# Kernel optimization log

Hardware: AMD Instinct MI355X
Metric: run time of the kernel (lower is better)

Reference implementation:

```python
import jax, jax.numpy as jnp
import numpy as np

EPS = 1e-12  # guard sqrt at zero distance


def setup_inputs() -> dict:
    key = jax.random.key(0)
    k1, k2 = jax.random.split(key)
    B, C, N = 4, 3, 8192
    predict_pc = jax.random.normal(k1, (B, C, N), dtype=jnp.float32)
    gt_pc = jax.random.normal(k2, (B, C, N), dtype=jnp.float32)
    return {"predict_pc": predict_pc, "gt_pc": gt_pc}


def reference(predict_pc, gt_pc):
    # predict_pc: [B, 3, Np], gt_pc: [B, 3, Ng]
    B = gt_pc.shape[0]
    Np = predict_pc.shape[2]
    Ng = gt_pc.shape[2]
    denom = B * (Ng + Np)

    # Pairwise Euclidean distances d[b, n, m] = ||predict[b,:,n] - gt[b,:,m]||
    # via the |p|^2 + |g|^2 - 2 p.g expansion (avoids [B,3,Np,Ng] intermediate).
    p2 = jnp.sum(predict_pc * predict_pc, axis=1)            # [B, Np]
    g2 = jnp.sum(gt_pc * gt_pc, axis=1)                      # [B, Ng]
    dot = jnp.einsum('bcn,bcm->bnm', predict_pc, gt_pc)      # [B, Np, Ng]
    d2 = p2[:, :, None] + g2[:, None, :] - 2.0 * dot         # [B, Np, Ng]
    d = jnp.sqrt(jnp.maximum(d2, EPS))

    # z: for each gt point, distance to nearest predicted point -> min over Np
    z = jnp.min(d, axis=1)   # [B, Ng]
    # z_2: for each predicted point, distance to nearest gt point -> min over Ng
    z2 = jnp.min(d, axis=2)  # [B, Np]

    loss = z.sum() / denom + z2.sum() / denom
    return loss
```

## Files before the change

kernel.cpp:

```cpp
#include <hip/hip_runtime.h>
#include <math.h>


#define B_       4
#define N_       8192
#define THREADS  256
#define RX       8
#define XB       (THREADS * RX)
#define XBLKS    (N_ / XB)
#define YSPLITS  32
#define YCHUNK   (N_ / YSPLITS)
#define NGROUPS  (2 * B_ * XBLKS)
#define POISON   0xAAAAAAAAu

typedef float v2f __attribute__((ext_vector_type(2)));

__device__ __forceinline__ v2f pk_fma(v2f a, v2f b, v2f c) {
    v2f d;
    asm("v_pk_fma_f32 %0, %1, %2, %3" : "=v"(d) : "v"(a), "v"(b), "v"(c));
    return d;
}


__global__ __launch_bounds__(THREADS)
void chamfer_fused_kernel(const float* __restrict__ P, const float* __restrict__ G,
                          unsigned* __restrict__ mins, unsigned* __restrict__ gcnt,
                          unsigned* __restrict__ fcnt, float* __restrict__ gsum,
                          float* __restrict__ out)
{
    __shared__ float4 ytile[2 * (YCHUNK / 2)];
    __shared__ float red[THREADS];
    __shared__ unsigned s_ticket;

    const int t      = threadIdx.x;
    const int xblk   = blockIdx.x;
    const int ysplit = blockIdx.y;
    const int bz     = blockIdx.z;
    const int pass   = bz >> 2;
    const int b      = bz & 3;
    const int gid    = bz * XBLKS + xblk;

    const float* Xb = (pass ? G : P) + (size_t)b * 3 * N_;
    const float* Yb = (pass ? P : G) + (size_t)b * 3 * N_;

    const int ybase = ysplit * YCHUNK;
    if (t < YCHUNK / 2) {
        const int n0 = ybase + 2 * t;
        float2 x01 = *(const float2*)&Yb[n0];
        float2 y01 = *(const float2*)&Yb[N_ + n0];
        float2 z01 = *(const float2*)&Yb[2 * N_ + n0];
        float w0 = fmaf(x01.x, x01.x, fmaf(y01.x, y01.x, z01.x * z01.x));
        float w1 = fmaf(x01.y, x01.y, fmaf(y01.y, y01.y, z01.y * z01.y));
        ytile[2 * t]     = make_float4(x01.x, x01.y, y01.x, y01.y);
        ytile[2 * t + 1] = make_float4(z01.x, z01.y, w0, w1);
    }

    const int xbase = xblk * XB;
    v2f m2x2[RX], m2y2[RX], m2z2[RX];
    float p2[RX], mn[RX];
#pragma unroll
    for (int r = 0; r < RX; ++r) {
        const int n = xbase + r * THREADS + t;
        float px = Xb[n];
        float py = Xb[N_ + n];
        float pz = Xb[2 * N_ + n];
        p2[r]   = fmaf(px, px, fmaf(py, py, pz * pz));
        float ax = -2.0f * px, ay = -2.0f * py, az = -2.0f * pz;
        m2x2[r] = (v2f){ax, ax};
        m2y2[r] = (v2f){ay, ay};
        m2z2[r] = (v2f){az, az};
        mn[r]   = 3.4e38f;
    }
    __syncthreads();

#pragma unroll 2
    for (int jj = 0; jj < YCHUNK / 2; ++jj) {
        float4 a4 = ytile[2 * jj];
        float4 b4 = ytile[2 * jj + 1];
        v2f gx2 = (v2f){a4.x, a4.y};
        v2f gy2 = (v2f){a4.z, a4.w};
        v2f gz2 = (v2f){b4.x, b4.y};
        v2f gw2 = (v2f){b4.z, b4.w};
#pragma unroll
        for (int r = 0; r < RX; ++r) {
            v2f s = pk_fma(m2z2[r], gz2, gw2);
            s = pk_fma(m2y2[r], gy2, s);
            s = pk_fma(m2x2[r], gx2, s);
            mn[r] = fminf(fminf(mn[r], s.x), s.y);
        }
    }

    unsigned* mybase = mins + (size_t)(pass * B_ + b) * N_ + xbase;
#pragma unroll
    for (int r = 0; r < RX; ++r) {
        float v = fmaxf(mn[r] + p2[r], 1e-12f);
        atomicMin(&mybase[r * THREADS + t], __float_as_uint(v));
    }

    __syncthreads();
    if (t == 0) {
        __threadfence();
        s_ticket = atomicAdd(&gcnt[gid], 1u);
    }
    __syncthreads();
    if (s_ticket != POISON + (unsigned)(YSPLITS - 1)) return;

    __threadfence();
    const uint4* vmin = (const uint4*)(mins + (size_t)(pass * B_ + b) * N_ + xbase);
    uint4 q0 = vmin[t];
    uint4 q1 = vmin[THREADS + t];
    float a = sqrtf(__uint_as_float(q0.x)) + sqrtf(__uint_as_float(q0.y))
            + sqrtf(__uint_as_float(q0.z)) + sqrtf(__uint_as_float(q0.w))
            + sqrtf(__uint_as_float(q1.x)) + sqrtf(__uint_as_float(q1.y))
            + sqrtf(__uint_as_float(q1.z)) + sqrtf(__uint_as_float(q1.w));
    red[t] = a;
    __syncthreads();
    for (int off = 128; off > 0; off >>= 1) {
        if (t < off) red[t] += red[t + off];
        __syncthreads();
    }
    if (t == 0) {
        gsum[gid] = red[0];
        __threadfence();
        s_ticket = atomicAdd(fcnt, 1u);
    }
    __syncthreads();
    if (s_ticket != POISON + (unsigned)(NGROUPS - 1)) return;

    __threadfence();
    red[t] = (t < NGROUPS) ? gsum[t] : 0.0f;
    __syncthreads();
    for (int off = 128; off > 0; off >>= 1) {
        if (t < off) red[t] += red[t + off];
        __syncthreads();
    }
    if (t == 0) out[0] = red[0] * (1.0f / 65536.0f);
}

extern "C" void kernel_launch(void* const* d_in, const int* in_sizes, int n_in,
                              void* d_out, int out_size, void* d_ws, size_t ws_size,
                              hipStream_t stream)
{
    const float* P = (const float*)d_in[0];
    const float* G = (const float*)d_in[1];
    float* out = (float*)d_out;

    unsigned* w    = (unsigned*)d_ws;
    unsigned* mins = w;
    unsigned* gcnt = w + 65536;
    unsigned* fcnt = w + 65600;
    float*    gsum = (float*)(w + 65664);

    dim3 grid(XBLKS, YSPLITS, 2 * B_);
    chamfer_fused_kernel<<<grid, THREADS, 0, stream>>>(P, G, mins, gcnt, fcnt, gsum, out);
}
```

Baseline: 97.96 us.

## Split chamfer into pack, sweep, and reduce kernels with global-memory Y streaming

Adds a multi-kernel path: a pack kernel precomputes interleaved Y records with squared norms, a sweep kernel streams those records from global memory with register prefetch and fewer X points per thread, and writes per-split partial minima. Two reduction kernels then take minima, apply sqrt, and sum, replacing atomics and ticket counters. The fused atomic kernel remains as a fallback when the workspace is too small. This trades per-block LDS staging and atomics for more launches, a large partial buffer, and lower per-thread reuse.

```diff
diff --git a/kernel.cpp b/kernel.cpp
--- a/kernel.cpp
+++ b/kernel.cpp
@@ -5,13 +5,6 @@
 #define B_       4
 #define N_       8192
 #define THREADS  256
-#define RX       8
-#define XB       (THREADS * RX)
-#define XBLKS    (N_ / XB)
-#define YSPLITS  32
-#define YCHUNK   (N_ / YSPLITS)
-#define NGROUPS  (2 * B_ * XBLKS)
-#define POISON   0xAAAAAAAAu
 
 typedef float v2f __attribute__((ext_vector_type(2)));
 
@@ -21,45 +14,57 @@
     return d;
 }
 
-
-__global__ __launch_bounds__(THREADS)
-void chamfer_fused_kernel(const float* __restrict__ P, const float* __restrict__ G,
-                          unsigned* __restrict__ mins, unsigned* __restrict__ gcnt,
-                          unsigned* __restrict__ fcnt, float* __restrict__ gsum,
-                          float* __restrict__ out)
-{
-    __shared__ float4 ytile[2 * (YCHUNK / 2)];
-    __shared__ float red[THREADS];
-    __shared__ unsigned s_ticket;
-
+#define RX1      2
+#define XB1      (THREADS * RX1)
+#define XBLKS1   (N_ / XB1)
+#define YSPL1    16
+#define YREC     (N_ / 2 / YSPL1)
+#define NPB      (2 * B_)
+#define NREC_PB  (N_ / 2)
+
+#define OFF_PACKED   0
+#define OFF_PARTIAL  262144
+#define OFF_GSUM2    1310720
+#define WORDS_NEED   1310976
+
+__global__ __launch_bounds__(THREADS)
+void chamfer_pack_kernel(const float* __restrict__ P, const float* __restrict__ G,
+                         float4* __restrict__ packed)
+{
+    const int g  = blockIdx.x * THREADS + threadIdx.x;
+    const int pb = g >> 12;
+    const int j  = g & 4095;
+    const int pass = pb >> 2, b = pb & 3;
+    const float* Yb = (pass ? P : G) + (size_t)b * 3 * N_;
+    const int n0 = 2 * j;
+    float2 x01 = *(const float2*)&Yb[n0];
+    float2 y01 = *(const float2*)&Yb[N_ + n0];
+    float2 z01 = *(const float2*)&Yb[2 * N_ + n0];
+    float w0 = fmaf(x01.x, x01.x, fmaf(y01.x, y01.x, z01.x * z01.x));
+    float w1 = fmaf(x01.y, x01.y, fmaf(y01.y, y01.y, z01.y * z01.y));
+    packed[2 * (size_t)g]     = make_float4(x01.x, x01.y, y01.x, y01.y);
+    packed[2 * (size_t)g + 1] = make_float4(z01.x, z01.y, w0, w1);
+}
+
+__global__ __launch_bounds__(THREADS)
+void chamfer_sweep_kernel(const float* __restrict__ P, const float* __restrict__ G,
+                          const float4* __restrict__ packed,
+                          float* __restrict__ partial)
+{
     const int t      = threadIdx.x;
     const int xblk   = blockIdx.x;
     const int ysplit = blockIdx.y;
     const int bz     = blockIdx.z;
     const int pass   = bz >> 2;
     const int b      = bz & 3;
-    const int gid    = bz * XBLKS + xblk;
 
     const float* Xb = (pass ? G : P) + (size_t)b * 3 * N_;
-    const float* Yb = (pass ? P : G) + (size_t)b * 3 * N_;
-
-    const int ybase = ysplit * YCHUNK;
-    if (t < YCHUNK / 2) {
-        const int n0 = ybase + 2 * t;
-        float2 x01 = *(const float2*)&Yb[n0];
-        float2 y01 = *(const float2*)&Yb[N_ + n0];
-        float2 z01 = *(const float2*)&Yb[2 * N_ + n0];
-        float w0 = fmaf(x01.x, x01.x, fmaf(y01.x, y01.x, z01.x * z01.x));
-        float w1 = fmaf(x01.y, x01.y, fmaf(y01.y, y01.y, z01.y * z01.y));
-        ytile[2 * t]     = make_float4(x01.x, x01.y, y01.x, y01.y);
-        ytile[2 * t + 1] = make_float4(z01.x, z01.y, w0, w1);
-    }
-
-    const int xbase = xblk * XB;
-    v2f m2x2[RX], m2y2[RX], m2z2[RX];
-    float p2[RX], mn[RX];
-#pragma unroll
-    for (int r = 0; r < RX; ++r) {
+    const int xbase = xblk * XB1;
+
+    v2f m2x2[RX1], m2y2[RX1], m2z2[RX1];
+    float p2[RX1], mn[RX1];
+#pragma unroll
+    for (int r = 0; r < RX1; ++r) {
         const int n = xbase + r * THREADS + t;
         float px = Xb[n];
         float py = Xb[N_ + n];
@@ -71,10 +76,130 @@
         m2z2[r] = (v2f){az, az};
         mn[r]   = 3.4e38f;
     }
-    __syncthreads();
-
+
+    const float4* rec = packed + 2 * ((size_t)bz * NREC_PB + ysplit * YREC);
+    float4 a0 = rec[0], b0 = rec[1];
+    float4 a1 = rec[2], b1 = rec[3];
 #pragma unroll 2
-    for (int jj = 0; jj < YCHUNK / 2; ++jj) {
+    for (int jj = 0; jj < YREC; ++jj) {
+        float4 an = rec[2 * jj + 4];
+        float4 bn = rec[2 * jj + 5];
+        v2f gx2 = (v2f){a0.x, a0.y};
+        v2f gy2 = (v2f){a0.z, a0.w};
+        v2f gz2 = (v2f){b0.x, b0.y};
+        v2f gw2 = (v2f){b0.z, b0.w};
+#pragma unroll
+        for (int r = 0; r < RX1; ++r) {
+            v2f s = pk_fma(m2z2[r], gz2, gw2);
+            s = pk_fma(m2y2[r], gy2, s);
+            s = pk_fma(m2x2[r], gx2, s);
+            mn[r] = fminf(fminf(mn[r], s.x), s.y);
+        }
+        a0 = a1; b0 = b1; a1 = an; b1 = bn;
+    }
+
+    float* pout = partial + ((size_t)bz * YSPL1 + ysplit) * N_ + xbase;
+#pragma unroll
+    for (int r = 0; r < RX1; ++r)
+        pout[r * THREADS + t] = fmaxf(mn[r] + p2[r], 1e-12f);
+}
+
+__global__ __launch_bounds__(THREADS)
+void chamfer_reduce1_kernel(const float* __restrict__ partial,
+                            float* __restrict__ gsum2)
+{
+    __shared__ float red[THREADS];
+    const int g  = blockIdx.x * THREADS + threadIdx.x;
+    const int pb = g >> 13;
+    const int x  = g & 8191;
+    const float* p = partial + (size_t)pb * YSPL1 * N_ + x;
+    float m = p[0];
+#pragma unroll
+    for (int ys = 1; ys < YSPL1; ++ys)
+        m = fminf(m, p[(size_t)ys * N_]);
+    red[threadIdx.x] = sqrtf(m);
+    __syncthreads();
+    for (int off = 128; off > 0; off >>= 1) {
+        if (threadIdx.x < off) red[threadIdx.x] += red[threadIdx.x + off];
+        __syncthreads();
+    }
+    if (threadIdx.x == 0) gsum2[blockIdx.x] = red[0];
+}
+
+__global__ __launch_bounds__(THREADS)
+void chamfer_final_kernel(const float* __restrict__ gsum2, float* __restrict__ out)
+{
+    __shared__ float red[THREADS];
+    red[threadIdx.x] = gsum2[threadIdx.x];
+    __syncthreads();
+    for (int off = 128; off > 0; off >>= 1) {
+        if (threadIdx.x < off) red[threadIdx.x] += red[threadIdx.x + off];
+        __syncthreads();
+    }
+    if (threadIdx.x == 0) out[0] = red[0] * (1.0f / 65536.0f);
+}
+
+#define LRX      8
+#define LXB      (THREADS * LRX)
+#define LXBLKS   (N_ / LXB)
+#define LYSPL    32
+#define LYCHUNK  (N_ / LYSPL)
+#define LNGROUPS (2 * B_ * LXBLKS)
+#define POISON   0xAAAAAAAAu
+
+__global__ __launch_bounds__(THREADS)
+void chamfer_fused_kernel(const float* __restrict__ P, const float* __restrict__ G,
+                          unsigned* __restrict__ mins, unsigned* __restrict__ gcnt,
+                          unsigned* __restrict__ fcnt, float* __restrict__ gsum,
+                          float* __restrict__ out)
+{
+    __shared__ float4 ytile[2 * (LYCHUNK / 2)];
+    __shared__ float red[THREADS];
+    __shared__ unsigned s_ticket;
+
+    const int t      = threadIdx.x;
+    const int xblk   = blockIdx.x;
+    const int ysplit = blockIdx.y;
+    const int bz     = blockIdx.z;
+    const int pass   = bz >> 2;
+    const int b      = bz & 3;
+    const int gid    = bz * LXBLKS + xblk;
+
+    const float* Xb = (pass ? G : P) + (size_t)b * 3 * N_;
+    const float* Yb = (pass ? P : G) + (size_t)b * 3 * N_;
+
+    const int ybase = ysplit * LYCHUNK;
+    if (t < LYCHUNK / 2) {
+        const int n0 = ybase + 2 * t;
+        float2 x01 = *(const float2*)&Yb[n0];
+        float2 y01 = *(const float2*)&Yb[N_ + n0];
+        float2 z01 = *(const float2*)&Yb[2 * N_ + n0];
+        float w0 = fmaf(x01.x, x01.x, fmaf(y01.x, y01.x, z01.x * z01.x));
+        float w1 = fmaf(x01.y, x01.y, fmaf(y01.y, y01.y, z01.y * z01.y));
+        ytile[2 * t]     = make_float4(x01.x, x01.y, y01.x, y01.y);
+        ytile[2 * t + 1] = make_float4(z01.x, z01.y, w0, w1);
+    }
+
+    const int xbase = xblk * LXB;
+    v2f m2x2[LRX], m2y2[LRX], m2z2[LRX];
+    float p2[LRX], mn[LRX];
+#pragma unroll
+    for (int r = 0; r < LRX; ++r) {
+        const int n = xbase + r * THREADS + t;
+        float px = Xb[n];
+        float py = Xb[N_ + n];
+        float pz = Xb[2 * N_ + n];
+        p2[r]   = fmaf(px, px, fmaf(py, py, pz * pz));
+        float ax = -2.0f * px, ay = -2.0f * py, az = -2.0f * pz;
+        m2x2[r] = (v2f){ax, ax};
+        m2y2[r] = (v2f){ay, ay};
+        m2z2[r] = (v2f){az, az};
+        mn[r]   = 3.4e38f;
+    }
+    __syncthreads();
+
+#pragma unroll 2
+    for (int jj = 0; jj < LYCHUNK / 2; ++jj) {
         float4 a4 = ytile[2 * jj];
         float4 b4 = ytile[2 * jj + 1];
         v2f gx2 = (v2f){a4.x, a4.y};
@@ -82,7 +207,7 @@
         v2f gz2 = (v2f){b4.x, b4.y};
         v2f gw2 = (v2f){b4.z, b4.w};
 #pragma unroll
-        for (int r = 0; r < RX; ++r) {
+        for (int r = 0; r < LRX; ++r) {
             v2f s = pk_fma(m2z2[r], gz2, gw2);
             s = pk_fma(m2y2[r], gy2, s);
             s = pk_fma(m2x2[r], gx2, s);
@@ -92,7 +217,7 @@
 
     unsigned* mybase = mins + (size_t)(pass * B_ + b) * N_ + xbase;
 #pragma unroll
-    for (int r = 0; r < RX; ++r) {
+    for (int r = 0; r < LRX; ++r) {
         float v = fmaxf(mn[r] + p2[r], 1e-12f);
         atomicMin(&mybase[r * THREADS + t], __float_as_uint(v));
     }
@@ -103,7 +228,7 @@
         s_ticket = atomicAdd(&gcnt[gid], 1u);
     }
     __syncthreads();
-    if (s_ticket != POISON + (unsigned)(YSPLITS - 1)) return;
+    if (s_ticket != POISON + (unsigned)(LYSPL - 1)) return;
 
     __threadfence();
     const uint4* vmin = (const uint4*)(mins + (size_t)(pass * B_ + b) * N_ + xbase);
@@ -125,10 +250,10 @@
         s_ticket = atomicAdd(fcnt, 1u);
     }
     __syncthreads();
-    if (s_ticket != POISON + (unsigned)(NGROUPS - 1)) return;
+    if (s_ticket != POISON + (unsigned)(LNGROUPS - 1)) return;
 
     __threadfence();
-    red[t] = (t < NGROUPS) ? gsum[t] : 0.0f;
+    red[t] = (t < LNGROUPS) ? gsum[t] : 0.0f;
     __syncthreads();
     for (int off = 128; off > 0; off >>= 1) {
         if (t < off) red[t] += red[t + off];
@@ -145,12 +270,22 @@
     const float* G = (const float*)d_in[1];
     float* out = (float*)d_out;
 
-    unsigned* w    = (unsigned*)d_ws;
-    unsigned* mins = w;
-    unsigned* gcnt = w + 65536;
-    unsigned* fcnt = w + 65600;
-    float*    gsum = (float*)(w + 65664);
-
-    dim3 grid(XBLKS, YSPLITS, 2 * B_);
-    chamfer_fused_kernel<<<grid, THREADS, 0, stream>>>(P, G, mins, gcnt, fcnt, gsum, out);
-}
+    if (ws_size >= (size_t)WORDS_NEED * 4) {
+        float*  wsf     = (float*)d_ws;
+        float4* packed  = (float4*)(wsf + OFF_PACKED);
+        float*  partial = wsf + OFF_PARTIAL;
+        float*  gsum2   = wsf + OFF_GSUM2;
+        chamfer_pack_kernel<<<dim3(128), THREADS, 0, stream>>>(P, G, packed);
+        chamfer_sweep_kernel<<<dim3(XBLKS1, YSPL1, 2 * B_), THREADS, 0, stream>>>(P, G, packed, partial);
+        chamfer_reduce1_kernel<<<dim3(256), THREADS, 0, stream>>>(partial, gsum2);
+        chamfer_final_kernel<<<dim3(1), THREADS, 0, stream>>>(gsum2, out);
+    } else {
+        unsigned* w    = (unsigned*)d_ws;
+        unsigned* mins = w;
+        unsigned* gcnt = w + 65536;
+        unsigned* fcnt = w + 65600;
+        float*    gsum = (float*)(w + 65664);
+        dim3 grid(LXBLKS, LYSPL, 2 * B_);
+        chamfer_fused_kernel<<<grid, THREADS, 0, stream>>>(P, G, mins, gcnt, fcnt, gsum, out);
+    }
+}
```

Result: slower. 128.7 us (+31.4%).
